# Kernel tuning notes

Hardware: AMD Instinct MI355X
Metric: run time of the kernel (lower is better)

## Reference

```python
import jax, jax.numpy as jnp
import numpy as np

DIM = 512
HEADS = 8
DIM_HEAD = 64
INNER = HEADS * DIM_HEAD  # 512
HIDDEN = 512 * 4          # mlp_dim * expansion
EPS = 1e-5
SCALE = DIM_HEAD ** -0.5


def layernorm(x, w, b):
    mu = jnp.mean(x, axis=-1, keepdims=True)
    var = jnp.var(x, axis=-1, keepdims=True)
    return (x - mu) * jax.lax.rsqrt(var + EPS) * w + b


def setup_inputs() -> dict:
    key = jax.random.key(0)
    ks = jax.random.split(key, 12)
    B, P, N = 2, 8, 1024  # P must equal HEADS (axis-swap bug in original rearrange)
    s = lambda k, shape, fan: jax.random.normal(k, shape, jnp.float32) * (fan ** -0.5)
    return {
        "x": jax.random.normal(ks[0], (B, P, N, DIM), jnp.float32),
        "ln0_w": jnp.ones((DIM,), jnp.float32),
        "ln0_b": jnp.zeros((DIM,), jnp.float32),
        "ln1_w": jnp.ones((DIM,), jnp.float32),
        "ln1_b": jnp.zeros((DIM,), jnp.float32),
        "w_qkv": s(ks[1], (DIM, 3 * INNER), DIM),
        "w_o": s(ks[2], (INNER, DIM), INNER),
        "b_o": jnp.zeros((DIM,), jnp.float32),
        "w1": s(ks[3], (DIM, HIDDEN), DIM),
        "b1": jnp.zeros((HIDDEN,), jnp.float32),
        "w2": s(ks[4], (HIDDEN, DIM), HIDDEN),
        "b2": jnp.zeros((DIM,), jnp.float32),
    }


def reference(x, ln0_w, ln0_b, ln1_w, ln1_b, w_qkv, w_o, b_o, w1, b1, w2, b2):
    B, P, N, _ = x.shape
    x = layernorm(x, ln0_w, ln0_b)  # outer block norm

    # ---- VisionAttention ----
    h = layernorm(x, ln1_w, ln1_b)
    qkv = h @ w_qkv                                    # [B,P,N,3*INNER]
    q, k, v = jnp.split(qkv, 3, axis=-1)
    def to_heads(t):  # [B,P,N,H*D] -> [B,H,P,N,D]
        return t.reshape(B, P, N, HEADS, DIM_HEAD).transpose(0, 3, 1, 2, 4)
    q, k, v = to_heads(q), to_heads(k), to_heads(v)
    dots = jnp.einsum("bhpnd,bhpmd->bhpnm", q, k) * SCALE  # full NxN scores
    attn = jax.nn.softmax(dots, axis=-1)
    out = jnp.einsum("bhpnm,bhpmd->bhpnd", attn, v)        # [B,H,P,N,D]
    # Faithful to buggy rearrange 'b p h n d -> b p n (h d)': swaps H and P axes.
    out = out.transpose(0, 1, 3, 2, 4).reshape(B, HEADS, N, P * DIM_HEAD)
    out = out @ w_o + b_o                                  # [B,H,N,DIM]
    x = out + x  # residual (valid because P == HEADS)

    # ---- MLP ----
    m = jax.nn.gelu(x @ w1 + b1, approximate=False) @ w2 + b2
    return m + x
```

## Files before the change

### kernel.cpp

```cpp
#include <hip/hip_runtime.h>
#include <hip/hip_bf16.h>
#include <math.h>

#define DIMV 512
#define NTOK 16384
#define NSEQ 1024
#define HEADSV 8
#define PPV 8
#define DHEAD 64
#define QKVW 1536
#define HIDV 2048
#define SC2 0.18033688011112042f

typedef unsigned short ushort;
typedef unsigned int uint;
typedef __attribute__((ext_vector_type(8))) short short8;
typedef __attribute__((ext_vector_type(8))) unsigned short ushort8;
typedef __attribute__((ext_vector_type(4))) unsigned short ushortx4;
typedef __attribute__((ext_vector_type(4))) float floatx4;

__device__ __forceinline__ float bf2f(ushort u){
  union { unsigned int i; float f; } c; c.i = ((unsigned int)u) << 16; return c.f;
}
__device__ __forceinline__ ushort f2bf(float f){
  union { float f; unsigned int i; } c; c.f = f;
  unsigned int u = c.i + 0x7fffu + ((c.i >> 16) & 1u);
  return (ushort)(u >> 16);
}
__device__ __forceinline__ void async_copy16(const void* gptr, void* lptr){
  __builtin_amdgcn_global_load_lds((const __attribute__((address_space(1))) void*)gptr,
                                   (__attribute__((address_space(3))) void*)lptr, 16, 0, 0);
}
__device__ __forceinline__ float fast_gelu(float x){
  float u = x * (2.3022084f + 0.1029435f * x * x);
  return x * __builtin_amdgcn_rcpf(1.f + exp2f(-u));
}

__device__ __forceinline__ void wave_reduce2(float& a, float& b){
  #pragma unroll
  for (int off = 32; off > 0; off >>= 1){
    a += __shfl_down(a, off, 64);
    b += __shfl_down(b, off, 64);
  }
}

__device__ __forceinline__ void wtrans_body(const float* __restrict__ W,
    __hip_bfloat16* __restrict__ Wt, int K, int N, int bx, int by, int t,
    float* tile ){
  int bn = bx * 32, bk = by * 32;
  int tx = t & 31, ty = t >> 5;
  #pragma unroll
  for (int i = 0; i < 32; i += 8)
    tile[(ty + i) * 33 + tx] = W[(size_t)(bk + ty + i) * N + bn + tx];
  __syncthreads();
  #pragma unroll
  for (int i = 0; i < 32; i += 8)
    Wt[(size_t)(bn + ty + i) * K + bk + tx] = __float2bfloat16(tile[tx * 33 + ty + i]);
}

__global__ __launch_bounds__(256) void prep_kernel(const float* __restrict__ x,
    const float* __restrict__ w0, const float* __restrict__ b0,
    const float* __restrict__ w1ln, const float* __restrict__ b1ln,
    __hip_bfloat16* __restrict__ x1, __hip_bfloat16* __restrict__ h,
    const float* __restrict__ wqkv, __hip_bfloat16* __restrict__ wqkvT,
    const float* __restrict__ wo,   __hip_bfloat16* __restrict__ woT,
    const float* __restrict__ w1,   __hip_bfloat16* __restrict__ w1T,
    const float* __restrict__ w2,   __hip_bfloat16* __restrict__ w2T){
  __shared__ float smem[32 * 33];
  int bid = blockIdx.x;
  int t = threadIdx.x;
  if (bid >= NTOK){
    int r = bid - NTOK;
    if (r < 768)        wtrans_body(wqkv, wqkvT, 512, 1536, r % 48, r / 48, t, smem);
    else if (r < 1024){ r -= 768;  wtrans_body(wo, woT, 512, 512,  r % 16, r / 16, t, smem); }
    else if (r < 2048){ r -= 1024; wtrans_body(w1, w1T, 512, 2048, r % 64, r / 64, t, smem); }
    else             { r -= 2048; wtrans_body(w2, w2T, 2048, 512, r % 16, r / 16, t, smem); }
    return;
  }
  float* sm = smem;
  size_t row = bid;
  const float2* xr = (const float2*)(x + row * DIMV);
  float2 v = xr[t];
  float s = v.x + v.y;
  float sq = v.x * v.x + v.y * v.y;
  wave_reduce2(s, sq);
  int wid = t >> 6, lane = t & 63;
  if (lane == 0){ sm[wid] = s; sm[8 + wid] = sq; }
  __syncthreads();
  s  = sm[0] + sm[1] + sm[2] + sm[3];
  sq = sm[8] + sm[9] + sm[10] + sm[11];
  float mu = s * (1.f / DIMV);
  float var = sq * (1.f / DIMV) - mu * mu;
  float r = rsqrtf(var + 1e-5f);
  float2 ww = ((const float2*)w0)[t];
  float2 bb = ((const float2*)b0)[t];
  float2 y;
  y.x = (v.x - mu) * r * ww.x + bb.x;
  y.y = (v.y - mu) * r * ww.y + bb.y;
  ushort2 xb; xb.x = f2bf(y.x); xb.y = f2bf(y.y);
  ((ushort2*)(x1 + row * DIMV))[t] = xb;
  float s2 = y.x + y.y, sq2 = y.x * y.x + y.y * y.y;
  wave_reduce2(s2, sq2);
  __syncthreads();
  if (lane == 0){ sm[wid] = s2; sm[8 + wid] = sq2; }
  __syncthreads();
  s2  = sm[0] + sm[1] + sm[2] + sm[3];
  sq2 = sm[8] + sm[9] + sm[10] + sm[11];
  float mu2 = s2 * (1.f / DIMV);
  float var2 = sq2 * (1.f / DIMV) - mu2 * mu2;
  float r2 = rsqrtf(var2 + 1e-5f);
  float2 w1v = ((const float2*)w1ln)[t];
  float2 b1v = ((const float2*)b1ln)[t];
  float hx = (y.x - mu2) * r2 * w1v.x + b1v.x;
  float hy = (y.y - mu2) * r2 * w1v.y + b1v.y;
  ushort2 hb; hb.x = f2bf(hx); hb.y = f2bf(hy);
  ((ushort2*)(h + row * DIMV))[t] = hb;
}

template<int SWAP>
__global__ __launch_bounds__(256) void gemm_mfma(
    const __hip_bfloat16* __restrict__ A,
    const __hip_bfloat16* __restrict__ Bt,
    const float* __restrict__ bias,
    const __hip_bfloat16* __restrict__ Rb,
    float* __restrict__ Cf,
    __hip_bfloat16* __restrict__ Cb,
    ushort* __restrict__ vt,
    int M, int N, int K, int gx, int dogelu)
{
  __shared__ __hip_bfloat16 As[3][128 * 32];
  __shared__ __hip_bfloat16 Bs[3][128 * 32];
  int tid = threadIdx.x;
  int w = tid >> 6, l = tid & 63;

  int bid = blockIdx.x;
  int xcd = bid & 7, idx = bid >> 3;
  int xl = idx % gx, yl = idx / gx;
  size_t bm = (size_t)(xcd * 16 + yl) * 128;
  size_t bn = (size_t)xl * 128;
  int wm = (w & 1) * 64, wn = (w >> 1) * 64;

  int srow = w * 16 + (l >> 2);
  int gcs = ((l & 3) ^ (srow & 3)) * 8;
  const __hip_bfloat16* Ag0 = A + (bm + srow) * K + gcs;
  const __hip_bfloat16* Ag1 = A + (bm + 64 + srow) * K + gcs;
  const __hip_bfloat16* Bg0 = Bt + (bn + srow) * K + gcs;
  const __hip_bfloat16* Bg1 = Bt + (bn + 64 + srow) * K + gcs;
  int lo = srow * 32 + (l & 3) * 8;

  floatx4 acc[4][4] = {};
  int fm = l & 15;
  int quad = l >> 4;
  int cs = fm & 3;

  int nk = K >> 5;
  async_copy16(Ag0, &As[0][lo]);
  async_copy16(Ag1, &As[0][lo + 64 * 32]);
  async_copy16(Bg0, &Bs[0][lo]);
  async_copy16(Bg1, &Bs[0][lo + 64 * 32]);
  if (nk > 1){
    async_copy16(Ag0 + 32, &As[1][lo]);
    async_copy16(Ag1 + 32, &As[1][lo + 64 * 32]);
    async_copy16(Bg0 + 32, &Bs[1][lo]);
    async_copy16(Bg1 + 32, &Bs[1][lo + 64 * 32]);
  }

  int rb = 0;
  for (int it = 0; it < nk; ++it){
    if (it + 1 < nk)
      asm volatile("s_waitcnt vmcnt(4)\n\ts_barrier" ::: "memory");
    else
      asm volatile("s_waitcnt vmcnt(0)\n\ts_barrier" ::: "memory");
    if (it + 2 < nk){
      int wb = rb >= 1 ? rb - 1 : 2;
      int k0 = (it + 2) << 5;
      async_copy16(Ag0 + k0, &As[wb][lo]);
      async_copy16(Ag1 + k0, &As[wb][lo + 64 * 32]);
      async_copy16(Bg0 + k0, &Bs[wb][lo]);
      async_copy16(Bg1 + k0, &Bs[wb][lo + 64 * 32]);
    }
    const __hip_bfloat16* Ab = As[rb];
    const __hip_bfloat16* Bb = Bs[rb];
    short8 af[4], bf[4];
    #pragma unroll
    for (int i = 0; i < 4; i++){
      af[i] = *(const short8*)&Ab[(wm + i * 16 + fm) * 32 + ((quad ^ cs) * 8)];
      bf[i] = *(const short8*)&Bb[(wn + i * 16 + fm) * 32 + ((quad ^ cs) * 8)];
    }
    #pragma unroll
    for (int mi = 0; mi < 4; mi++)
      #pragma unroll
      for (int ni = 0; ni < 4; ni++){
        if (SWAP)
          acc[mi][ni] = __builtin_amdgcn_mfma_f32_16x16x32_bf16(bf[ni], af[mi], acc[mi][ni], 0, 0, 0);
        else
          acc[mi][ni] = __builtin_amdgcn_mfma_f32_16x16x32_bf16(af[mi], bf[ni], acc[mi][ni], 0, 0, 0);
      }
    rb = rb < 2 ? rb + 1 : 0;
  }

  int rq = quad * 4;
  if (SWAP){
    #pragma unroll
    for (int mi = 0; mi < 4; mi++){
      size_t row = bm + wm + mi * 16 + fm;
      size_t rbase = row * (size_t)N + bn + wn + rq;
      #pragma unroll
      for (int ni = 0; ni < 4; ni++){
        size_t idx2 = rbase + ni * 16;
        floatx4 v = acc[mi][ni];
        if (bias){
          floatx4 bv = *(const floatx4*)(bias + bn + wn + ni * 16 + rq);
          #pragma unroll
          for (int r2 = 0; r2 < 4; r2++) v[r2] += bv[r2];
        }
        if (dogelu){
          #pragma unroll
          for (int r2 = 0; r2 < 4; r2++) v[r2] = fast_gelu(v[r2]);
        }
        if (Rb){
          ushortx4 rbv = *(const ushortx4*)((const ushort*)Rb + idx2);
          #pragma unroll
          for (int r2 = 0; r2 < 4; r2++) v[r2] += bf2f(rbv[r2]);
        }
        if (Cb){
          ushortx4 ob;
          #pragma unroll
          for (int r2 = 0; r2 < 4; r2++) ob[r2] = f2bf(v[r2]);
          *(ushortx4*)((ushort*)Cb + idx2) = ob;
        } else {
          *(floatx4*)(Cf + idx2) = v;
        }
      }
    }
  } else {
    if (vt && bn >= 1024){
      int b = (int)(bm >> 13), p = (int)((bm >> 10) & 7);
      int n0 = (int)(bm & 1023) + wm + rq;
      int cbase = (int)bn + wn - 1024;
      #pragma unroll
      for (int ni = 0; ni < 4; ni++){
        int cc = cbase + ni * 16 + fm;
        int hh = cc >> 6, dd = cc & 63;
        ushort* vdst = vt + ((size_t)((b * 8 + hh) * 8 + p)) * 65536 + (size_t)dd * 1024;
        #pragma unroll
        for (int mi = 0; mi < 4; mi++){
          ushortx4 v4;
          v4[0] = f2bf(acc[mi][ni][0]); v4[1] = f2bf(acc[mi][ni][1]);
          v4[2] = f2bf(acc[mi][ni][2]); v4[3] = f2bf(acc[mi][ni][3]);
          *(ushortx4*)(vdst + n0 + mi * 16) = v4;
        }
      }
    } else if (Cb){
      float scl = (vt && bn < 512) ? SC2 : 1.f;
      #pragma unroll
      for (int ni = 0; ni < 4; ni++){
        size_t col = bn + wn + ni * 16 + fm;
        float bv = bias ? bias[col] : 0.f;
        #pragma unroll
        for (int mi = 0; mi < 4; mi++){
          #pragma unroll
          for (int r2 = 0; r2 < 4; r2++){
            size_t row = bm + wm + mi * 16 + rq + r2;
            float v = acc[mi][ni][r2];
            if (vt) v *= scl;
            v += bv;
            if (dogelu) v = fast_gelu(v);
            size_t idx2 = row * N + col;
            if (Rb) v += bf2f(((const ushort*)Rb)[idx2]);
            ((ushort*)Cb)[idx2] = f2bf(v);
          }
        }
      }
    } else {
      #pragma unroll
      for (int ni = 0; ni < 4; ni++){
        size_t col = bn + wn + ni * 16 + fm;
        float bv = bias ? bias[col] : 0.f;
        #pragma unroll
        for (int mi = 0; mi < 4; mi++){
          #pragma unroll
          for (int r2 = 0; r2 < 4; r2++){
            size_t row = bm + wm + mi * 16 + rq + r2;
            float v = acc[mi][ni][r2] + bv;
            if (dogelu) v = fast_gelu(v);
            size_t idx2 = row * N + col;
            if (Rb) v += bf2f(((const ushort*)Rb)[idx2]);
            Cf[idx2] = v;
          }
        }
      }
    }
  }
}

__global__ __launch_bounds__(256, 4) void attn_mfma(const __hip_bfloat16* __restrict__ qkvp,
                                                    const ushort* __restrict__ vt,
                                                    __hip_bfloat16* __restrict__ outp){
  __shared__ ushort Ks[2][64 * 64];
  __shared__ ushort Vs[2][64 * 64];
  __shared__ ushort Ps[4][32 * 32];
  int tid = threadIdx.x;
  int w = tid >> 6, l = tid & 63;
  int r15 = l & 15, quad = l >> 4, fq = quad * 8;
  int slice = blockIdx.x & 127;
  int qc = blockIdx.x >> 7;
  int b = slice >> 6, hh = (slice >> 3) & 7, p = slice & 7;
  const ushort* base = (const ushort*)qkvp + (size_t)(b * PPV + p) * NSEQ * QKVW;
  const ushort* kb = base + 512 + hh * DHEAD;
  const ushort* vb = vt + (size_t)slice * 65536;

  int s0 = w * 64 + l, s1 = 256 + w * 64 + l;
  int row0 = s0 >> 3, row1 = s1 >> 3;
  int gc0 = (s0 & 7) ^ (row0 & 7), gc1 = (s1 & 7) ^ (row1 & 7);
  const ushort* kp0 = kb + (size_t)row0 * QKVW + gc0 * 8;
  const ushort* kp1 = kb + (size_t)row1 * QKVW + gc1 * 8;
  const ushort* vp0 = vb + (size_t)row0 * 1024 + gc0 * 8;
  const ushort* vp1 = vb + (size_t)row1 * 1024 + gc1 * 8;

  async_copy16(kp0, &Ks[0][s0 * 8]);
  async_copy16(kp1, &Ks[0][s1 * 8]);
  async_copy16(vp0, &Vs[0][s0 * 8]);
  async_copy16(vp1, &Vs[0][s1 * 8]);

  int q0 = qc * 128 + w * 32;
  short8 qf[2][2];
  #pragma unroll
  for (int mi = 0; mi < 2; mi++)
    #pragma unroll
    for (int kk = 0; kk < 2; kk++)
      qf[mi][kk] = *(const short8*)(base + (size_t)(q0 + mi * 16 + r15) * QKVW + hh * DHEAD + kk * 32 + fq);

  floatx4 o[2][4] = {};
  floatx4 lacc[2] = {};
  short8 ones;
  #pragma unroll
  for (int j = 0; j < 8; j++) ones[j] = (short)0x3F80;

  int sw = r15 & 7;
  int swp = (r15 & 3) << 3;
  ushort* PsW = Ps[w];

  for (int it = 0; it < NSEQ / 64; ++it){
    int cur = it & 1;
    asm volatile("s_waitcnt vmcnt(0)\n\ts_barrier" ::: "memory");
    if (it + 1 < NSEQ / 64){
      int nxt = cur ^ 1;
      kp0 += 64 * QKVW; kp1 += 64 * QKVW; vp0 += 64; vp1 += 64;
      async_copy16(kp0, &Ks[nxt][s0 * 8]);
      async_copy16(kp1, &Ks[nxt][s1 * 8]);
      async_copy16(vp0, &Vs[nxt][s0 * 8]);
      async_copy16(vp1, &Vs[nxt][s1 * 8]);
    }
    const ushort* Kb = Ks[cur];
    const ushort* Vb = Vs[cur];

    short8 pf[2][2];
    #pragma unroll
    for (int kk = 0; kk < 2; kk++){
      #pragma unroll
      for (int nn = 0; nn < 2; nn++){
        int ni = kk * 2 + nn;
        int rb2 = (ni * 16 + r15) * 64;
        short8 kf0 = *(const short8*)&Kb[rb2 + (quad ^ sw) * 8];
        short8 kf1 = *(const short8*)&Kb[rb2 + ((4 + quad) ^ sw) * 8];
        floatx4 sA = {}, sB = {};
        sA = __builtin_amdgcn_mfma_f32_16x16x32_bf16(kf0, qf[0][0], sA, 0, 0, 0);
        sA = __builtin_amdgcn_mfma_f32_16x16x32_bf16(kf1, qf[0][1], sA, 0, 0, 0);
        sB = __builtin_amdgcn_mfma_f32_16x16x32_bf16(kf0, qf[1][0], sB, 0, 0, 0);
        sB = __builtin_amdgcn_mfma_f32_16x16x32_bf16(kf1, qf[1][1], sB, 0, 0, 0);
        int wc = (nn * 16 + quad * 4) ^ swp;
        union { float f; uint u; } e0, e1, e2, e3;
        uint2 pk;
        e0.f = exp2f(sA[0]); e1.f = exp2f(sA[1]);
        e2.f = exp2f(sA[2]); e3.f = exp2f(sA[3]);
        pk.x = __builtin_amdgcn_perm(e1.u, e0.u, 0x07060302u);
        pk.y = __builtin_amdgcn_perm(e3.u, e2.u, 0x07060302u);
        *(uint2*)&PsW[r15 * 32 + wc] = pk;
        e0.f = exp2f(sB[0]); e1.f = exp2f(sB[1]);
        e2.f = exp2f(sB[2]); e3.f = exp2f(sB[3]);
        pk.x = __builtin_amdgcn_perm(e1.u, e0.u, 0x07060302u);
        pk.y = __builtin_amdgcn_perm(e3.u, e2.u, 0x07060302u);
        *(uint2*)&PsW[(16 + r15) * 32 + wc] = pk;
      }
      asm volatile("s_waitcnt lgkmcnt(0)" ::: "memory");
      pf[0][kk] = *(const short8*)&PsW[r15 * 32 + (fq ^ swp)];
      pf[1][kk] = *(const short8*)&PsW[(16 + r15) * 32 + (fq ^ swp)];
      asm volatile("s_waitcnt lgkmcnt(0)" ::: "memory");
    }

    #pragma unroll
    for (int mi = 0; mi < 2; mi++)
      #pragma unroll
      for (int kk = 0; kk < 2; kk++)
        lacc[mi] = __builtin_amdgcn_mfma_f32_16x16x32_bf16(ones, pf[mi][kk], lacc[mi], 0, 0, 0);

    #pragma unroll
    for (int dj = 0; dj < 4; dj++){
      int d = dj * 16 + r15;
      short8 vf0 = *(const short8*)&Vb[d * 64 + ((quad) ^ sw) * 8];
      short8 vf1 = *(const short8*)&Vb[d * 64 + ((4 + quad) ^ sw) * 8];
      #pragma unroll
      for (int mi = 0; mi < 2; mi++){
        o[mi][dj] = __builtin_amdgcn_mfma_f32_16x16x32_bf16(vf0, pf[mi][0], o[mi][dj], 0, 0, 0);
        o[mi][dj] = __builtin_amdgcn_mfma_f32_16x16x32_bf16(vf1, pf[mi][1], o[mi][dj], 0, 0, 0);
      }
    }
  }

  #pragma unroll
  for (int mi = 0; mi < 2; mi++){
    float inv = __builtin_amdgcn_rcpf(lacc[mi][0]);
    size_t n = q0 + mi * 16 + r15;
    ushort* orow = (ushort*)outp + ((size_t)((b * HEADSV + hh) * NSEQ + n)) * DIMV + p * DHEAD + quad * 4;
    #pragma unroll
    for (int dj = 0; dj < 4; dj++){
      ushortx4 ov;
      #pragma unroll
      for (int r = 0; r < 4; r++) ov[r] = f2bf(o[mi][dj][r] * inv);
      *(ushortx4*)(orow + dj * 16) = ov;
    }
  }
}

extern "C" void kernel_launch(void* const* d_in, const int* in_sizes, int n_in,
                              void* d_out, int out_size, void* d_ws, size_t ws_size,
                              hipStream_t stream){
  (void)in_sizes; (void)n_in; (void)out_size; (void)ws_size;
  const float* x    = (const float*)d_in[0];
  const float* lw0  = (const float*)d_in[1];
  const float* lb0  = (const float*)d_in[2];
  const float* lw1  = (const float*)d_in[3];
  const float* lb1  = (const float*)d_in[4];
  const float* wqkv = (const float*)d_in[5];
  const float* wo   = (const float*)d_in[6];
  const float* bo   = (const float*)d_in[7];
  const float* w1   = (const float*)d_in[8];
  const float* b1   = (const float*)d_in[9];
  const float* w2   = (const float*)d_in[10];
  const float* b2   = (const float*)d_in[11];
  float* out = (float*)d_out;
  char* ws = (char*)d_ws;
  const size_t MB = 1024 * 1024;

  __hip_bfloat16* x1b  = (__hip_bfloat16*)(ws);
  ushort* vtbuf        = (ushort*)(ws + 32 * MB);
  __hip_bfloat16* x2b  = (__hip_bfloat16*)(ws + 64 * MB);
  __hip_bfloat16* wqkvT= (__hip_bfloat16*)(ws + 80 * MB);
  __hip_bfloat16* woT  = (__hip_bfloat16*)(ws + 82 * MB);
  __hip_bfloat16* w1T  = (__hip_bfloat16*)(ws + 83 * MB);
  __hip_bfloat16* w2T  = (__hip_bfloat16*)(ws + 85 * MB);
  __hip_bfloat16* hB   = (__hip_bfloat16*)(ws + 88 * MB);
  __hip_bfloat16* attnB= hB;
  __hip_bfloat16* qkvB = (__hip_bfloat16*)(ws + 104 * MB);
  __hip_bfloat16* tB   = (__hip_bfloat16*)(ws + 88 * MB);

  prep_kernel<<<NTOK + 3072, 256, 0, stream>>>(
      x, lw0, lb0, lw1, lb1, x1b, hB,
      wqkv, wqkvT, wo, woT, w1, w1T, w2, w2T);

  gemm_mfma<0><<<(QKVW / 128) * 128, 256, 0, stream>>>(
      hB, wqkvT, nullptr, nullptr, nullptr, qkvB, vtbuf,
      NTOK, QKVW, DIMV, QKVW / 128, 0);

  attn_mfma<<<1024, 256, 0, stream>>>(qkvB, vtbuf, attnB);

  gemm_mfma<1><<<(DIMV / 128) * 128, 256, 0, stream>>>(
      attnB, woT, bo, x1b, nullptr, x2b, nullptr,
      NTOK, DIMV, DIMV, DIMV / 128, 0);

  gemm_mfma<1><<<(HIDV / 128) * 128, 256, 0, stream>>>(
      x2b, w1T, b1, nullptr, nullptr, tB, nullptr,
      NTOK, HIDV, DIMV, HIDV / 128, 1);

  gemm_mfma<1><<<(DIMV / 128) * 128, 256, 0, stream>>>(
      tB, w2T, b2, x2b, out, nullptr, nullptr,
      NTOK, DIMV, HIDV, DIMV / 128, 0);
}
```

Baseline: 366.8 us.

## Add 256x256-tile 8-wave GEMM with phased prefetch for QKV and MLP-up

Adds a new GEMM kernel using 256x256 output tiles, 512 threads (8 waves), a 64-wide K step with double-buffered swizzled LDS, and async global-to-LDS copies staggered across four compute phases with raised wave priority around the MFMA blocks. It replaces the 128x128 GEMM for the QKV projection (including the V-transpose and Q-scale epilogue) and for the MLP up-projection with GELU. The aim is more data reuse per tile and better overlap of loads with MFMA work. In exchange it uses far more LDS and accumulator registers per block, leaves fewer blocks to spread across CUs, and the now-unused QKV epilogue paths are removed from the old kernel.

```diff
diff --git a/kernel.cpp b/kernel.cpp
--- a/kernel.cpp
+++ b/kernel.cpp
@@ -118,6 +118,179 @@
 }
 
 template<int SWAP>
+__global__ __launch_bounds__(512, 2) void gemm_8p(
+    const __hip_bfloat16* __restrict__ A,
+    const __hip_bfloat16* __restrict__ Bt,
+    const float* __restrict__ bias,
+    __hip_bfloat16* __restrict__ Cb,
+    ushort* __restrict__ vt,
+    int M, int N, int K, int gx, int dogelu)
+{
+  __shared__ __hip_bfloat16 As[2][256 * 64];
+  __shared__ __hip_bfloat16 Bs[2][256 * 64];
+  int tid = threadIdx.x;
+  int l = tid & 63, w = tid >> 6;
+  int wr = w >> 2, wc = w & 3;
+  int fm = l & 15, quad = l >> 4;
+
+  int bid = blockIdx.x;
+  int xcd = bid & 7, idx = bid >> 3;
+  int xl = idx % gx, yl = idx / gx;
+  size_t bm = (size_t)(xcd * 8 + yl) * 256;
+  size_t bn = (size_t)xl * 256;
+
+  int sr = tid >> 3;
+  int sc = ((tid & 7) ^ (sr & 7)) * 8;
+  const __hip_bfloat16* Ab0 = A + (bm + sr) * (size_t)K + sc;
+  const __hip_bfloat16* Bb0 = Bt + (bn + sr) * (size_t)K + sc;
+  int ldst = tid * 8;
+
+  int nk = K >> 6;
+
+  #pragma unroll
+  for (int j = 0; j < 4; j++)
+    async_copy16(Ab0 + (size_t)j * 64 * K, &As[0][j * 4096 + ldst]);
+  #pragma unroll
+  for (int j = 0; j < 4; j++)
+    async_copy16(Bb0 + (size_t)j * 64 * K, &Bs[0][j * 4096 + ldst]);
+
+  floatx4 acc[8][4] = {};
+
+  int arow = wr * 128 + fm;
+  int brow = wc * 64 + fm;
+  int cx = fm & 7;
+
+  for (int t = 0; t < nk; ++t){
+    int cur = t & 1, nxt = cur ^ 1;
+    const __hip_bfloat16* Asrc = Ab0 + (size_t)(t + 1) * 64;
+    const __hip_bfloat16* Bsrc = Bb0 + (size_t)(t + 1) * 64;
+    const __hip_bfloat16* Ac = As[cur];
+    const __hip_bfloat16* Bc = Bs[cur];
+    short8 bf[4][2], af[2][2];
+
+    if (t + 1 < nk){
+      async_copy16(Asrc, &As[nxt][ldst]);
+      async_copy16(Asrc + (size_t)64 * K, &As[nxt][4096 + ldst]);
+      asm volatile("s_waitcnt vmcnt(2)\n\ts_barrier" ::: "memory");
+    } else {
+      asm volatile("s_waitcnt vmcnt(0)\n\ts_barrier" ::: "memory");
+    }
+    #pragma unroll
+    for (int ci = 0; ci < 4; ci++)
+      #pragma unroll
+      for (int kb = 0; kb < 2; kb++)
+        bf[ci][kb] = *(const short8*)&Bc[(brow + ci * 16) * 64 + ((kb * 4 + quad) ^ cx) * 8];
+    #pragma unroll
+    for (int i = 0; i < 2; i++)
+      #pragma unroll
+      for (int kb = 0; kb < 2; kb++)
+        af[i][kb] = *(const short8*)&Ac[(arow + i * 16) * 64 + ((kb * 4 + quad) ^ cx) * 8];
+    __builtin_amdgcn_s_setprio(1);
+    #pragma unroll
+    for (int i = 0; i < 2; i++)
+      #pragma unroll
+      for (int ci = 0; ci < 4; ci++)
+        #pragma unroll
+        for (int kb = 0; kb < 2; kb++){
+          if (SWAP)
+            acc[i][ci] = __builtin_amdgcn_mfma_f32_16x16x32_bf16(bf[ci][kb], af[i][kb], acc[i][ci], 0, 0, 0);
+          else
+            acc[i][ci] = __builtin_amdgcn_mfma_f32_16x16x32_bf16(af[i][kb], bf[ci][kb], acc[i][ci], 0, 0, 0);
+        }
+    __builtin_amdgcn_s_setprio(0);
+    asm volatile("s_barrier" ::: "memory");
+
+    #pragma unroll
+    for (int p = 1; p < 4; p++){
+      #pragma unroll
+      for (int i = 0; i < 2; i++)
+        #pragma unroll
+        for (int kb = 0; kb < 2; kb++)
+          af[i][kb] = *(const short8*)&Ac[(arow + (p * 2 + i) * 16) * 64 + ((kb * 4 + quad) ^ cx) * 8];
+      if (t + 1 < nk){
+        if (p == 1){
+          async_copy16(Asrc + (size_t)128 * K, &As[nxt][2 * 4096 + ldst]);
+          async_copy16(Asrc + (size_t)192 * K, &As[nxt][3 * 4096 + ldst]);
+        } else if (p == 2){
+          async_copy16(Bsrc, &Bs[nxt][ldst]);
+          async_copy16(Bsrc + (size_t)64 * K, &Bs[nxt][4096 + ldst]);
+        } else {
+          async_copy16(Bsrc + (size_t)128 * K, &Bs[nxt][2 * 4096 + ldst]);
+          async_copy16(Bsrc + (size_t)192 * K, &Bs[nxt][3 * 4096 + ldst]);
+        }
+      }
+      asm volatile("s_barrier" ::: "memory");
+      __builtin_amdgcn_s_setprio(1);
+      #pragma unroll
+      for (int i = 0; i < 2; i++)
+        #pragma unroll
+        for (int ci = 0; ci < 4; ci++)
+          #pragma unroll
+          for (int kb = 0; kb < 2; kb++){
+            if (SWAP)
+              acc[p * 2 + i][ci] = __builtin_amdgcn_mfma_f32_16x16x32_bf16(bf[ci][kb], af[i][kb], acc[p * 2 + i][ci], 0, 0, 0);
+            else
+              acc[p * 2 + i][ci] = __builtin_amdgcn_mfma_f32_16x16x32_bf16(af[i][kb], bf[ci][kb], acc[p * 2 + i][ci], 0, 0, 0);
+          }
+      __builtin_amdgcn_s_setprio(0);
+      asm volatile("s_barrier" ::: "memory");
+    }
+  }
+
+  if (SWAP){
+    #pragma unroll
+    for (int ri = 0; ri < 8; ri++){
+      size_t row = bm + wr * 128 + ri * 16 + fm;
+      size_t rbase = row * (size_t)N + bn + wc * 64 + quad * 4;
+      #pragma unroll
+      for (int ci = 0; ci < 4; ci++){
+        floatx4 v = acc[ri][ci];
+        if (bias){
+          floatx4 bv = *(const floatx4*)(bias + bn + wc * 64 + ci * 16 + quad * 4);
+          #pragma unroll
+          for (int r2 = 0; r2 < 4; r2++) v[r2] += bv[r2];
+        }
+        if (dogelu){
+          #pragma unroll
+          for (int r2 = 0; r2 < 4; r2++) v[r2] = fast_gelu(v[r2]);
+        }
+        ushortx4 ob;
+        #pragma unroll
+        for (int r2 = 0; r2 < 4; r2++) ob[r2] = f2bf(v[r2]);
+        *(ushortx4*)((ushort*)Cb + rbase + ci * 16) = ob;
+      }
+    }
+  } else {
+    int b = (int)(bm >> 13), p = (int)((bm >> 10) & 7);
+    int n0 = (int)(bm & 1023) + wr * 128 + quad * 4;
+    #pragma unroll
+    for (int ci = 0; ci < 4; ci++){
+      int col = (int)bn + wc * 64 + ci * 16 + fm;
+      if (col >= 1024){
+        int cc = col - 1024, hh = cc >> 6, dd = cc & 63;
+        ushort* vdst = vt + ((size_t)((b * 8 + hh) * 8 + p)) * 65536 + (size_t)dd * 1024 + n0;
+        #pragma unroll
+        for (int ri = 0; ri < 8; ri++){
+          ushortx4 v4;
+          v4[0] = f2bf(acc[ri][ci][0]); v4[1] = f2bf(acc[ri][ci][1]);
+          v4[2] = f2bf(acc[ri][ci][2]); v4[3] = f2bf(acc[ri][ci][3]);
+          *(ushortx4*)(vdst + ri * 16) = v4;
+        }
+      } else {
+        float scl = (col < 512) ? SC2 : 1.f;
+        #pragma unroll
+        for (int ri = 0; ri < 8; ri++){
+          size_t rowb = bm + wr * 128 + ri * 16 + quad * 4;
+          #pragma unroll
+          for (int r2 = 0; r2 < 4; r2++)
+            ((ushort*)Cb)[(rowb + r2) * (size_t)N + col] = f2bf(acc[ri][ci][r2] * scl);
+        }
+      }
+    }
+  }
+}
+
+template<int SWAP>
 __global__ __launch_bounds__(256) void gemm_mfma(
     const __hip_bfloat16* __restrict__ A,
     const __hip_bfloat16* __restrict__ Bt,
@@ -234,60 +407,20 @@
       }
     }
   } else {
-    if (vt && bn >= 1024){
-      int b = (int)(bm >> 13), p = (int)((bm >> 10) & 7);
-      int n0 = (int)(bm & 1023) + wm + rq;
-      int cbase = (int)bn + wn - 1024;
-      #pragma unroll
-      for (int ni = 0; ni < 4; ni++){
-        int cc = cbase + ni * 16 + fm;
-        int hh = cc >> 6, dd = cc & 63;
-        ushort* vdst = vt + ((size_t)((b * 8 + hh) * 8 + p)) * 65536 + (size_t)dd * 1024;
+    #pragma unroll
+    for (int ni = 0; ni < 4; ni++){
+      size_t col = bn + wn + ni * 16 + fm;
+      float bv = bias ? bias[col] : 0.f;
+      #pragma unroll
+      for (int mi = 0; mi < 4; mi++){
         #pragma unroll
-        for (int mi = 0; mi < 4; mi++){
-          ushortx4 v4;
-          v4[0] = f2bf(acc[mi][ni][0]); v4[1] = f2bf(acc[mi][ni][1]);
-          v4[2] = f2bf(acc[mi][ni][2]); v4[3] = f2bf(acc[mi][ni][3]);
-          *(ushortx4*)(vdst + n0 + mi * 16) = v4;
-        }
-      }
-    } else if (Cb){
-      float scl = (vt && bn < 512) ? SC2 : 1.f;
-      #pragma unroll
-      for (int ni = 0; ni < 4; ni++){
-        size_t col = bn + wn + ni * 16 + fm;
-        float bv = bias ? bias[col] : 0.f;
-        #pragma unroll
-        for (int mi = 0; mi < 4; mi++){
-          #pragma unroll
-          for (int r2 = 0; r2 < 4; r2++){
-            size_t row = bm + wm + mi * 16 + rq + r2;
-            float v = acc[mi][ni][r2];
-            if (vt) v *= scl;
-            v += bv;
-            if (dogelu) v = fast_gelu(v);
-            size_t idx2 = row * N + col;
-            if (Rb) v += bf2f(((const ushort*)Rb)[idx2]);
-            ((ushort*)Cb)[idx2] = f2bf(v);
-          }
-        }
-      }
-    } else {
-      #pragma unroll
-      for (int ni = 0; ni < 4; ni++){
-        size_t col = bn + wn + ni * 16 + fm;
-        float bv = bias ? bias[col] : 0.f;
-        #pragma unroll
-        for (int mi = 0; mi < 4; mi++){
-          #pragma unroll
-          for (int r2 = 0; r2 < 4; r2++){
-            size_t row = bm + wm + mi * 16 + rq + r2;
-            float v = acc[mi][ni][r2] + bv;
-            if (dogelu) v = fast_gelu(v);
-            size_t idx2 = row * N + col;
-            if (Rb) v += bf2f(((const ushort*)Rb)[idx2]);
-            Cf[idx2] = v;
-          }
+        for (int r2 = 0; r2 < 4; r2++){
+          size_t row = bm + wm + mi * 16 + rq + r2;
+          float v = acc[mi][ni][r2] + bv;
+          if (dogelu) v = fast_gelu(v);
+          size_t idx2 = row * N + col;
+          if (Rb) v += bf2f(((const ushort*)Rb)[idx2]);
+          Cf[idx2] = v;
         }
       }
     }
@@ -459,9 +592,8 @@
       x, lw0, lb0, lw1, lb1, x1b, hB,
       wqkv, wqkvT, wo, woT, w1, w1T, w2, w2T);
 
-  gemm_mfma<0><<<(QKVW / 128) * 128, 256, 0, stream>>>(
-      hB, wqkvT, nullptr, nullptr, nullptr, qkvB, vtbuf,
-      NTOK, QKVW, DIMV, QKVW / 128, 0);
+  gemm_8p<0><<<384, 512, 0, stream>>>(
+      hB, wqkvT, nullptr, qkvB, vtbuf, NTOK, QKVW, DIMV, 6, 0);
 
   attn_mfma<<<1024, 256, 0, stream>>>(qkvB, vtbuf, attnB);
 
@@ -469,9 +601,8 @@
       attnB, woT, bo, x1b, nullptr, x2b, nullptr,
       NTOK, DIMV, DIMV, DIMV / 128, 0);
 
-  gemm_mfma<1><<<(HIDV / 128) * 128, 256, 0, stream>>>(
-      x2b, w1T, b1, nullptr, nullptr, tB, nullptr,
-      NTOK, HIDV, DIMV, HIDV / 128, 1);
+  gemm_8p<1><<<512, 512, 0, stream>>>(
+      x2b, w1T, b1, tB, nullptr, NTOK, HIDV, DIMV, 8, 1);
 
   gemm_mfma<1><<<(DIMV / 128) * 128, 256, 0, stream>>>(
       tB, w2T, b2, x2b, out, nullptr, nullptr,
```

Measured after the change: 353.9 us. 3.5% less time.
